# Kernel optimization log

Measured on AMD Instinct MI355X. Metric: run time of the kernel, lower is better.

## Reference

```python
import jax, jax.numpy as jnp
import numpy as np

N = 32768   # nodes
E = 524288  # edges (avg degree 16)
D = 128     # in_channels == num_hidden_channels
H = 4       # attention heads
C = D // H  # per-head out channels
R = 5       # num_relations
BS = 8192   # batch_size (output rows)
NEG = 0.2   # GATv2Conv leaky_relu negative slope


def segment_softmax(alpha, dst, n):
    amax = jax.lax.stop_gradient(jax.ops.segment_max(alpha, dst, num_segments=n))
    amax = jnp.where(jnp.isfinite(amax), amax, 0.0)
    a = jnp.exp(alpha - amax[dst])
    denom = jax.ops.segment_sum(a, dst, num_segments=n)
    return a / (denom[dst] + 1e-16)


def rel_edge_features(x, src, dst, Rmat, etype):
    # cat(src, dst) @ R[etype], computed per-relation to avoid gathering [E,2D,D]
    e = jnp.concatenate([x[src], x[dst]], axis=1)  # [E, 2D]
    out = jnp.zeros((e.shape[0], Rmat.shape[-1]), e.dtype)
    for r in range(Rmat.shape[0]):
        out = out + jnp.where((etype == r)[:, None], e @ Rmat[r], 0.0)
    return jax.nn.gelu(out, approximate=False)


def gatv2_conv(x, src, dst, edge_attr, Wl, bl, We, att, bias):
    # share_weights=True: x_l == x_r
    n = x.shape[0]
    xl = (x @ Wl + bl).reshape(n, H, C)
    m = xl[src] + xl[dst] + (edge_attr @ We).reshape(-1, H, C)  # [E,H,C]
    alpha = jnp.einsum('ehc,hc->eh', jax.nn.leaky_relu(m, NEG), att)
    alpha = segment_softmax(alpha, dst, n)
    msg = xl[src] * alpha[..., None]
    return jax.ops.segment_sum(msg, dst, num_segments=n).reshape(n, H * C) + bias


def setup_inputs():
    key = jax.random.key(0)
    ks = jax.random.split(key, 18)
    s = 0.05
    f32 = jnp.float32
    return {
        'embs': jax.random.normal(ks[0], (N, D), f32),
        'edge_index': jax.random.randint(ks[1], (2, E), 0, N),
        'edge_type': jax.random.randint(ks[2], (E,), 0, R),
        'rel_matrices': jax.random.normal(ks[3], (1, 2, R, 2 * D, D), f32) * s,
        'lin_l_w0': jax.random.normal(ks[4], (D, H * C), f32) * s,
        'lin_l_b0': jnp.zeros((H * C,), f32),
        'lin_edge_w0': jax.random.normal(ks[5], (D, H * C), f32) * s,
        'att0': jax.random.normal(ks[6], (H, C), f32) * s,
        'bias0': jnp.zeros((H * C,), f32),
        'lin_l_w1': jax.random.normal(ks[7], (D, H * C), f32) * s,
        'lin_l_b1': jnp.zeros((H * C,), f32),
        'lin_edge_w1': jax.random.normal(ks[8], (D, H * C), f32) * s,
        'att1': jax.random.normal(ks[9], (H, C), f32) * s,
        'bias1': jnp.zeros((H * C,), f32),
        'out_w': jax.random.normal(ks[10], (D, D), f32) * s,
        'out_b': jnp.zeros((D,), f32),
        'ln_g': jnp.ones((D,), f32),
        'ln_b': jnp.zeros((D,), f32),
        'batch_size': BS,
    }


def reference(embs, edge_index, edge_type, rel_matrices,
              lin_l_w0, lin_l_b0, lin_edge_w0, att0, bias0,
              lin_l_w1, lin_l_b1, lin_edge_w1, att1, bias1,
              out_w, out_b, ln_g, ln_b, batch_size):
    src, dst = edge_index[0], edge_index[1]
    x = embs
    # inner layer 0 (dropout no-op in eval)
    ea = rel_edge_features(x, src, dst, rel_matrices[0, 0], edge_type)
    x = gatv2_conv(x, src, dst, ea, lin_l_w0, lin_l_b0, lin_edge_w0, att0, bias0)
    x = jax.nn.gelu(x, approximate=False)
    # inner layer 1 (last -> no activation)
    ea = rel_edge_features(x, src, dst, rel_matrices[0, 1], edge_type)
    x = gatv2_conv(x, src, dst, ea, lin_l_w1, lin_l_b1, lin_edge_w1, att1, bias1)
    # output head: Linear -> LayerNorm(eps=1e-12) -> Dropout(no-op)
    y = x[:batch_size] @ out_w + out_b
    mu = y.mean(-1, keepdims=True)
    var = y.var(-1, keepdims=True)
    return (y - mu) / jnp.sqrt(var + 1e-12) * ln_g + ln_b
```

## Files before the change

### kernel.cpp

```cpp
#include <hip/hip_runtime.h>
#include <hip/hip_bf16.h>

typedef __hip_bfloat16 bf16;
typedef __attribute__((ext_vector_type(8))) short s8v;
typedef __attribute__((ext_vector_type(4))) float f4v;
typedef __attribute__((ext_vector_type(2))) float f2v;
typedef unsigned short u16;
typedef unsigned int u32;
typedef unsigned char u8;
typedef long long i64;

#define NN 32768
#define NE 524288
#define D 128
#define H 4
#define C 32
#define R 5
#define BS 8192

__device__ __forceinline__ u16 f2bs(float x) { bf16 h = __float2bfloat16(x); return *(u16*)&h; }
__device__ __forceinline__ float bflo(u32 u) { return __uint_as_float(u << 16); }
__device__ __forceinline__ float bfhi(u32 u) { return __uint_as_float(u & 0xffff0000u); }
__device__ __forceinline__ u32 pack2r(float a, float b) {
    u32 ua = __float_as_uint(a) + 0x8000u;
    u32 ub = __float_as_uint(b) + 0x8000u;
    return __builtin_amdgcn_perm(ub, ua, 0x07060302u);
}
__device__ __forceinline__ u16 rnd16(float a) {
    return (u16)((__float_as_uint(a) + 0x8000u) >> 16);
}
__device__ __forceinline__ float gelu_f(float x) {
    return 0.5f * x * (1.f + erff(x * 0.7071067811865475f));
}
__device__ __forceinline__ f2v gelu_pk(f2v x) {
    f2v t;
    t.x = fminf(fmaxf(x.x, -4.f), 4.f);
    t.y = fminf(fmaxf(x.y, -4.f), 4.f);
    f2v s = t * t;
    f2v h = __builtin_elementwise_fma(s, (f2v)1.53421e-5f, (f2v)-7.13918e-4f);
    h = __builtin_elementwise_fma(s, h, (f2v)0.0129194f);
    h = __builtin_elementwise_fma(s, h, (f2v)-0.1207967f);
    h = __builtin_elementwise_fma(s, h, (f2v)0.794118f);
    f2v e = t * h;
    f2v hx = x * 0.5f;
    return __builtin_elementwise_fma(hx, e, hx);
}
template <int CTRL>
__device__ __forceinline__ float dpp_add(float v) {
    int t = __builtin_amdgcn_update_dpp(0, __float_as_int(v), CTRL, 0xf, 0xf, true);
    return v + __int_as_float(t);
}
__device__ __forceinline__ float rsum16(float v) {
    v = dpp_add<0x128>(v);
    v = dpp_add<0x124>(v);
    v = dpp_add<0x122>(v);
    v = dpp_add<0x121>(v);
    return v;
}

__device__ u16      g_x[NN * D];
__device__ float    g_araw[NE * H];
__device__ u8       g_P8[R * NN * D];
__device__ u8       g_Q8[R * NN * D];
__device__ u16      g_xl[NN * D];
__device__ u8       g_xl8[NN * D];
__device__ u16      g_WnF[26 * 2048 * 8];
__device__ int      g_cnt[NN];
__device__ int      g_cur[NN];
__device__ int      g_off[NN + 1];
__device__ int      g_se[NE];
__device__ int      g_de[NE];
__device__ int      g_re[NE];

__global__ void k_cvt(const float* __restrict__ e) {
    int i = blockIdx.x * 256 + threadIdx.x;
    float2 v = *(const float2*)&e[(size_t)i * 2];
    ((u32*)g_x)[i] = pack2r(v.x, v.y);
}

__global__ void k_zcnt() {
    int i = blockIdx.x * 256 + threadIdx.x;
    g_cnt[i] = 0; g_cur[i] = 0;
}
__global__ void k_count(const int* __restrict__ ei) {
    int i = blockIdx.x * 256 + threadIdx.x;
    atomicAdd(&g_cnt[ei[NE + i]], 1);
}
__global__ void k_scan() {
    __shared__ int sums[1024];
    const int t = threadIdx.x;
    const int base = t * 32;
    int local[32];
    int s = 0;
#pragma unroll
    for (int i = 0; i < 32; ++i) { local[i] = s; s += g_cnt[base + i]; }
    sums[t] = s;
    __syncthreads();
    for (int off = 1; off < 1024; off <<= 1) {
        int v = (t >= off) ? sums[t - off] : 0;
        __syncthreads();
        sums[t] += v;
        __syncthreads();
    }
    int chunkoff = (t == 0) ? 0 : sums[t - 1];
#pragma unroll
    for (int i = 0; i < 32; ++i) g_off[base + i] = chunkoff + local[i];
    if (t == 1023) g_off[NN] = sums[1023];
}
__global__ void k_scatter(const int* __restrict__ ei, const int* __restrict__ et) {
    int i = blockIdx.x * 256 + threadIdx.x;
    int d = ei[NE + i];
    int pos = g_off[d] + atomicAdd(&g_cur[d], 1);
    g_se[pos] = ei[i];
    g_de[pos] = d;
    g_re[pos] = et[i];
}

__global__ void k_prep(const float* __restrict__ Wl, const float* __restrict__ Rm,
                       const float* __restrict__ We, const float* __restrict__ Ow,
                       int base) {
    int f = blockIdx.x * 256 + threadIdx.x;
    int y = blockIdx.y;
    const float* src;
    if (y == 0) src = Wl;
    else if (y <= R) src = Rm + (size_t)(y - 1) * 2 * D * D;
    else if (y <= 2 * R) src = Rm + (size_t)(y - 1 - R) * 2 * D * D + D * D;
    else if (y == 11) src = We;
    else src = Ow;
    int lane = f & 63, nt = (f >> 6) & 7, s = f >> 9;
    int n = nt * 16 + (lane & 15);
    int ks = s * 32 + (lane >> 4) * 8;
    u16 tmp[8];
#pragma unroll
    for (int j = 0; j < 8; ++j) tmp[j] = f2bs(src[(size_t)(ks + j) * D + n]);
    *(uint4*)&g_WnF[((size_t)(base + y) * 2048 + f) * 8] = *(uint4*)tmp;
}

__global__ __launch_bounds__(256) void k_node(const float* __restrict__ bl, int wbase) {
    const int tid = threadIdx.x;
    const int n0 = blockIdx.x * 64;
    const int wstart = blockIdx.y * 3;
    const int wend = (wstart + 3 < 11) ? wstart + 3 : 11;
    const int l = tid & 63, w = tid >> 6;
    const int mrow = l & 15, quad = l >> 4;
    const u16* xrow = g_x + (size_t)(n0 + w * 16 + mrow) * D;

    s8v a[4];
#pragma unroll
    for (int s = 0; s < 4; ++s) a[s] = *(const s8v*)&xrow[s * 32 + quad * 8];

    for (int wsel = wstart; wsel < wend; ++wsel) {
        const u16* BF = g_WnF + (size_t)(wbase + wsel) * 2048 * 8;
        f4v acc[8];
#pragma unroll
        for (int nt = 0; nt < 8; ++nt) acc[nt] = (f4v){0.f, 0.f, 0.f, 0.f};
#pragma unroll
        for (int s = 0; s < 4; ++s) {
#pragma unroll
            for (int nt = 0; nt < 8; ++nt) {
                s8v b = *(const s8v*)&BF[(size_t)((s * 8 + nt) * 64 + l) * 8];
                acc[nt] = __builtin_amdgcn_mfma_f32_16x16x32_bf16(a[s], b, acc[nt], 0, 0, 0);
            }
        }

        if (wsel == 0) {
#pragma unroll
            for (int nt = 0; nt < 8; ++nt) {
                int col = nt * 16 + mrow;
                float bias = bl[col];
                float v[4];
#pragma unroll
                for (int r = 0; r < 4; ++r) v[r] = acc[nt][r] + bias;
#pragma unroll
                for (int r = 0; r < 4; ++r) {
                    int row = n0 + w * 16 + quad * 4 + r;
                    g_xl[(size_t)row * D + col] = rnd16(v[r]);
                }
#pragma unroll
                for (int r = 0; r < 4; r += 2) {
                    u32 pk = __builtin_amdgcn_cvt_pk_fp8_f32(v[r], v[r + 1], 0, false);
                    int row = n0 + w * 16 + quad * 4 + r;
                    g_xl8[(size_t)row * D + col] = (u8)(pk & 0xffu);
                    g_xl8[(size_t)(row + 1) * D + col] = (u8)((pk >> 8) & 0xffu);
                }
            }
        } else {
            u8* out8 = (wsel <= R) ? g_P8 + (size_t)(wsel - 1) * NN * D
                                   : g_Q8 + (size_t)(wsel - 1 - R) * NN * D;
#pragma unroll
            for (int nt = 0; nt < 8; ++nt) {
                int col = nt * 16 + mrow;
#pragma unroll
                for (int r = 0; r < 4; r += 2) {
                    u32 pk = __builtin_amdgcn_cvt_pk_fp8_f32(acc[nt][r], acc[nt][r + 1], 0, false);
                    int row = n0 + w * 16 + quad * 4 + r;
                    out8[(size_t)row * D + col] = (u8)(pk & 0xffu);
                    out8[(size_t)(row + 1) * D + col] = (u8)((pk >> 8) & 0xffu);
                }
            }
        }
    }
}

__global__ __launch_bounds__(256) void k_edge(const float* __restrict__ att, int wbase) {
    const int tid = threadIdx.x;
    const int e0 = blockIdx.x * 64;
    const int l = tid & 63, w = tid >> 6;
    const int mrow = l & 15, quad = l >> 4;
    const int myrow = w * 16 + mrow;
    const u16* BF = g_WnF + (size_t)(wbase + 11) * 2048 * 8;

    const int se = g_se[e0 + myrow];
    const int de = g_de[e0 + myrow];
    const int re = g_re[e0 + myrow];

    const int pos8 = (mrow & 7) * 8;
    const i64 bev8 = (quad == (mrow >> 3))     ? (i64)(0x38LL << pos8) : 0LL;
    const i64 bod8 = (quad == 2 + (mrow >> 3)) ? (i64)(0x38LL << pos8) : 0LL;

    const u8* Prow = g_P8 + ((size_t)re * NN + se) * D;
    const u8* Qrow = g_Q8 + ((size_t)re * NN + de) * D;
    const u8* Xs = g_xl8 + (size_t)se * D;
    const u8* Xd = g_xl8 + (size_t)de * D;
    union { u32 u[4]; s8v v; } af[4];
    uint2 su[4], du[4];
#pragma unroll
    for (int s = 0; s < 4; ++s) {
        int c0 = s * 32 + quad * 8;
        uint2 pu = *(const uint2*)&Prow[c0];
        uint2 qu = *(const uint2*)&Qrow[c0];
        su[s] = *(const uint2*)&Xs[c0];
        du[s] = *(const uint2*)&Xd[c0];
        f2v pq0 = __builtin_amdgcn_cvt_pk_f32_fp8(pu.x, false) + __builtin_amdgcn_cvt_pk_f32_fp8(qu.x, false);
        f2v pq1 = __builtin_amdgcn_cvt_pk_f32_fp8(pu.x, true)  + __builtin_amdgcn_cvt_pk_f32_fp8(qu.x, true);
        f2v pq2 = __builtin_amdgcn_cvt_pk_f32_fp8(pu.y, false) + __builtin_amdgcn_cvt_pk_f32_fp8(qu.y, false);
        f2v pq3 = __builtin_amdgcn_cvt_pk_f32_fp8(pu.y, true)  + __builtin_amdgcn_cvt_pk_f32_fp8(qu.y, true);
        f2v g0 = gelu_pk(pq0), g1 = gelu_pk(pq1), g2 = gelu_pk(pq2), g3 = gelu_pk(pq3);
        af[s].u[0] = pack2r(g0.x, g0.y);
        af[s].u[1] = pack2r(g1.x, g1.y);
        af[s].u[2] = pack2r(g2.x, g2.y);
        af[s].u[3] = pack2r(g3.x, g3.y);
    }

    f4v acc[8];
#pragma unroll
    for (int nt = 0; nt < 8; ++nt) acc[nt] = (f4v){0.f, 0.f, 0.f, 0.f};
#pragma unroll
    for (int s = 0; s < 4; ++s) {
#pragma unroll
        for (int nt = 0; nt < 8; ++nt) {
            s8v b = *(const s8v*)&BF[(size_t)((s * 8 + nt) * 64 + l) * 8];
            acc[nt] = __builtin_amdgcn_mfma_f32_16x16x32_bf16(af[s].v, b, acc[nt], 0, 0, 0);
        }
        const i64 as = (i64)(((unsigned long long)su[s].y << 32) | su[s].x);
        const i64 ad = (i64)(((unsigned long long)du[s].y << 32) | du[s].x);
        acc[2 * s]     = __builtin_amdgcn_mfma_f32_16x16x32_fp8_fp8(as, bev8, acc[2 * s], 0, 0, 0);
        acc[2 * s]     = __builtin_amdgcn_mfma_f32_16x16x32_fp8_fp8(ad, bev8, acc[2 * s], 0, 0, 0);
        acc[2 * s + 1] = __builtin_amdgcn_mfma_f32_16x16x32_fp8_fp8(as, bod8, acc[2 * s + 1], 0, 0, 0);
        acc[2 * s + 1] = __builtin_amdgcn_mfma_f32_16x16x32_fp8_fp8(ad, bod8, acc[2 * s + 1], 0, 0, 0);
    }

    float hsum[4][4];
#pragma unroll
    for (int r = 0; r < 4; ++r)
#pragma unroll
        for (int h = 0; h < 4; ++h) hsum[r][h] = 0.f;
#pragma unroll
    for (int nt = 0; nt < 8; ++nt) {
        int col = nt * 16 + mrow;
        float av = att[col];
        int h = nt >> 1;
#pragma unroll
        for (int r = 0; r < 4; ++r) {
            float m = acc[nt][r];
            float lr = fmaxf(m, 0.2f * m);
            hsum[r][h] = fmaf(lr, av, hsum[r][h]);
        }
    }
#pragma unroll
    for (int r = 0; r < 4; ++r)
#pragma unroll
        for (int h = 0; h < 4; ++h) hsum[r][h] = rsum16(hsum[r][h]);
    if ((mrow & 3) == 0) {
        int r = mrow >> 2;
        float4 v = make_float4(__expf(fminf(hsum[r][0], 80.f)),
                               __expf(fminf(hsum[r][1], 80.f)),
                               __expf(fminf(hsum[r][2], 80.f)),
                               __expf(fminf(hsum[r][3], 80.f)));
        *(float4*)&g_araw[(size_t)(e0 + w * 16 + quad * 4 + r) * H] = v;
    }
}

__global__ __launch_bounds__(256) void k_gath(const float* __restrict__ bias,
                                              int do_gelu) {
    const int lane = threadIdx.x & 63;
    const int d = blockIdx.x * 4 + (threadIdx.x >> 6);
    const int off = g_off[d];
    const int deg = g_off[d + 1] - off;
    const int h = lane >> 4;

    const int* __restrict__ srcs = g_se + off;
    const float* __restrict__ ar = g_araw + (size_t)off * H + h;
    float a0 = 0.f, a1 = 0.f, dn = 0.f;
    int p = 0;
    for (; p + 8 <= deg; p += 8) {
        int ss[8];
#pragma unroll
        for (int j = 0; j < 8; ++j) ss[j] = srcs[p + j];
        u32 ww[8];
#pragma unroll
        for (int j = 0; j < 8; ++j) ww[j] = *(const u32*)&g_xl[(size_t)ss[j] * D + lane * 2];
        float cc[8];
#pragma unroll
        for (int j = 0; j < 8; ++j) cc[j] = ar[(p + j) * H];
#pragma unroll
        for (int j = 0; j < 8; ++j) {
            dn += cc[j];
            a0 = fmaf(bflo(ww[j]), cc[j], a0);
            a1 = fmaf(bfhi(ww[j]), cc[j], a1);
        }
    }
    for (; p + 4 <= deg; p += 4) {
        int s0 = srcs[p], s1 = srcs[p + 1], s2 = srcs[p + 2], s3 = srcs[p + 3];
        u32 w0 = *(const u32*)&g_xl[(size_t)s0 * D + lane * 2];
        u32 w1 = *(const u32*)&g_xl[(size_t)s1 * D + lane * 2];
        u32 w2 = *(const u32*)&g_xl[(size_t)s2 * D + lane * 2];
        u32 w3 = *(const u32*)&g_xl[(size_t)s3 * D + lane * 2];
        float c0 = ar[(p + 0) * H];
        float c1 = ar[(p + 1) * H];
        float c2 = ar[(p + 2) * H];
        float c3 = ar[(p + 3) * H];
        dn += (c0 + c1) + (c2 + c3);
        a0 = fmaf(bflo(w0), c0, a0); a1 = fmaf(bfhi(w0), c0, a1);
        a0 = fmaf(bflo(w1), c1, a0); a1 = fmaf(bfhi(w1), c1, a1);
        a0 = fmaf(bflo(w2), c2, a0); a1 = fmaf(bfhi(w2), c2, a1);
        a0 = fmaf(bflo(w3), c3, a0); a1 = fmaf(bfhi(w3), c3, a1);
    }
    for (; p < deg; ++p) {
        int s = srcs[p];
        u32 w = *(const u32*)&g_xl[(size_t)s * D + lane * 2];
        float cf = ar[p * H];
        dn += cf;
        a0 = fmaf(bflo(w), cf, a0);
        a1 = fmaf(bfhi(w), cf, a1);
    }
    const float inv = __builtin_amdgcn_rcpf(dn + 1e-16f);
    float v0 = a0 * inv + bias[lane * 2];
    float v1 = a1 * inv + bias[lane * 2 + 1];
    if (do_gelu) { v0 = gelu_f(v0); v1 = gelu_f(v1); }
    ((u32*)g_x)[(size_t)d * (D / 2) + lane] = pack2r(v0, v1);
}

__global__ __launch_bounds__(256) void k_head(const float* __restrict__ ob,
                                              const float* __restrict__ g,
                                              const float* __restrict__ b,
                                              float* __restrict__ out) {
    const int tid = threadIdx.x;
    const int r0 = blockIdx.x * 64;
    const int l = tid & 63, w = tid >> 6;
    const int mrow = l & 15, quad = l >> 4;
    const u16* xrow = g_x + (size_t)(r0 + w * 16 + mrow) * D;
    const u16* BF = g_WnF + (size_t)12 * 2048 * 8;

    f4v acc[8];
#pragma unroll
    for (int nt = 0; nt < 8; ++nt) acc[nt] = (f4v){0.f, 0.f, 0.f, 0.f};
#pragma unroll
    for (int s = 0; s < 4; ++s) {
        s8v a = *(const s8v*)&xrow[s * 32 + quad * 8];
#pragma unroll
        for (int nt = 0; nt < 8; ++nt) {
            s8v bb = *(const s8v*)&BF[(size_t)((s * 8 + nt) * 64 + l) * 8];
            acc[nt] = __builtin_amdgcn_mfma_f32_16x16x32_bf16(a, bb, acc[nt], 0, 0, 0);
        }
    }

    float sum[4] = {0.f, 0.f, 0.f, 0.f};
#pragma unroll
    for (int nt = 0; nt < 8; ++nt) {
        float obv = ob[nt * 16 + mrow];
#pragma unroll
        for (int r = 0; r < 4; ++r) {
            acc[nt][r] += obv;
            sum[r] += acc[nt][r];
        }
    }
    float mu[4];
#pragma unroll
    for (int r = 0; r < 4; ++r) mu[r] = rsum16(sum[r]) * (1.f / D);
    float sq[4] = {0.f, 0.f, 0.f, 0.f};
#pragma unroll
    for (int nt = 0; nt < 8; ++nt)
#pragma unroll
        for (int r = 0; r < 4; ++r) {
            float dv = acc[nt][r] - mu[r];
            sq[r] += dv * dv;
        }
    float rs[4];
#pragma unroll
    for (int r = 0; r < 4; ++r) rs[r] = rsqrtf(rsum16(sq[r]) * (1.f / D) + 1e-12f);
#pragma unroll
    for (int nt = 0; nt < 8; ++nt) {
        int col = nt * 16 + mrow;
        float gv = g[col], bv = b[col];
#pragma unroll
        for (int r = 0; r < 4; ++r) {
            int row = r0 + w * 16 + quad * 4 + r;
            out[(size_t)row * D + col] = (acc[nt][r] - mu[r]) * rs[r] * gv + bv;
        }
    }
}

extern "C" void kernel_launch(void* const* d_in, const int* in_sizes, int n_in,
                              void* d_out, int out_size, void* d_ws, size_t ws_size,
                              hipStream_t stream) {
    (void)in_sizes; (void)n_in; (void)out_size; (void)d_ws; (void)ws_size;
    const float* embs = (const float*)d_in[0];
    const int*   ei   = (const int*)d_in[1];
    const int*   et   = (const int*)d_in[2];
    const float* rel  = (const float*)d_in[3];
    const float* wl[2]   = { (const float*)d_in[4],  (const float*)d_in[9]  };
    const float* bl[2]   = { (const float*)d_in[5],  (const float*)d_in[10] };
    const float* we[2]   = { (const float*)d_in[6],  (const float*)d_in[11] };
    const float* attw[2] = { (const float*)d_in[7],  (const float*)d_in[12] };
    const float* bs[2]   = { (const float*)d_in[8],  (const float*)d_in[13] };
    const float* ow  = (const float*)d_in[14];
    const float* ob  = (const float*)d_in[15];
    const float* lng = (const float*)d_in[16];
    const float* lnb = (const float*)d_in[17];
    float* out = (float*)d_out;

    k_cvt<<<NN * D / 512, 256, 0, stream>>>(embs);

    for (int l = 0; l < 2; ++l) {
        const float* Rm = rel + (size_t)l * R * 2 * D * D;
        k_prep<<<dim3(2048 / 256, 13), 256, 0, stream>>>(wl[l], Rm, we[l], ow, l * 13);
    }

    k_zcnt<<<NN / 256, 256, 0, stream>>>();
    k_count<<<NE / 256, 256, 0, stream>>>(ei);
    k_scan<<<1, 1024, 0, stream>>>();
    k_scatter<<<NE / 256, 256, 0, stream>>>(ei, et);

    for (int l = 0; l < 2; ++l) {
        k_node<<<dim3(NN / 64, 4), 256, 0, stream>>>(bl[l], l * 13);
        k_edge<<<NE / 64, 256, 0, stream>>>(attw[l], l * 13);
        k_gath<<<NN / 4, 256, 0, stream>>>(bs[l], l == 0 ? 1 : 0);
    }

    k_head<<<BS / 64, 256, 0, stream>>>(ob, lng, lnb, out);
}
```

Measured before the change: 478.3 us.

## Sort edges by relation type before edge kernel for gather locality

Adds a stable counting sort that groups CSR-ordered edges by relation type: per-block histograms, a global scan, and a scatter that ranks edges within each block. The edge kernel then reads edges in relation-grouped order, so the P8/Q8 rows it gathers come from a single relation slab at a time. Scores are written back to their original CSR position through a packed index. This adds three small preprocessing kernels, including an O(256) per-thread rank loop, and an indirect scattered store of the attention scores, in exchange for better cache locality on the relation-table gathers.

Measured after the change: 491.9 us. +2.8%, slower.

```diff
diff --git a/kernel.cpp b/kernel.cpp
--- a/kernel.cpp
+++ b/kernel.cpp
@@ -17,6 +17,7 @@
 #define C 32
 #define R 5
 #define BS 8192
+#define NB 2048
 
 __device__ __forceinline__ u16 f2bs(float x) { bf16 h = __float2bfloat16(x); return *(u16*)&h; }
 __device__ __forceinline__ float bflo(u32 u) { return __uint_as_float(u << 16); }
@@ -71,6 +72,10 @@
 __device__ int      g_se[NE];
 __device__ int      g_de[NE];
 __device__ int      g_re[NE];
+__device__ int      g_bh[R * NB];
+__device__ int      g_hse[NE];
+__device__ int      g_hde[NE];
+__device__ u32      g_hpr[NE];
 
 __global__ void k_cvt(const float* __restrict__ e) {
     int i = blockIdx.x * 256 + threadIdx.x;
@@ -114,6 +119,52 @@
     g_se[pos] = ei[i];
     g_de[pos] = d;
     g_re[pos] = et[i];
+}
+
+__global__ void k_phist() {
+    __shared__ int h[R];
+    const int t = threadIdx.x, b = blockIdx.x;
+    if (t < R) h[t] = 0;
+    __syncthreads();
+    atomicAdd(&h[g_re[b * 256 + t]], 1);
+    __syncthreads();
+    if (t < R) g_bh[t * NB + b] = h[t];
+}
+__global__ void k_pscan() {
+    __shared__ int sums[1024];
+    const int t = threadIdx.x;
+    const int base = t * 10;
+    int local[10];
+    int s = 0;
+#pragma unroll
+    for (int i = 0; i < 10; ++i) { local[i] = s; s += g_bh[base + i]; }
+    sums[t] = s;
+    __syncthreads();
+    for (int off = 1; off < 1024; off <<= 1) {
+        int v = (t >= off) ? sums[t - off] : 0;
+        __syncthreads();
+        sums[t] += v;
+        __syncthreads();
+    }
+    int chunkoff = (t == 0) ? 0 : sums[t - 1];
+#pragma unroll
+    for (int i = 0; i < 10; ++i) g_bh[base + i] = chunkoff + local[i];
+}
+__global__ void k_pscat() {
+    __shared__ u8 lre[256];
+    __shared__ int bofs[R];
+    const int t = threadIdx.x, b = blockIdx.x;
+    const int i = b * 256 + t;
+    const int re = g_re[i];
+    lre[t] = (u8)re;
+    if (t < R) bofs[t] = g_bh[t * NB + b];
+    __syncthreads();
+    int rank = 0;
+    for (int j = 0; j < t; ++j) rank += (lre[j] == (u8)re);
+    const int pos = bofs[re] + rank;
+    g_hse[pos] = g_se[i];
+    g_hde[pos] = g_de[i];
+    g_hpr[pos] = ((u32)re << 24) | (u32)i;
 }
 
 __global__ void k_prep(const float* __restrict__ Wl, const float* __restrict__ Rm,
@@ -210,9 +261,9 @@
     const int myrow = w * 16 + mrow;
     const u16* BF = g_WnF + (size_t)(wbase + 11) * 2048 * 8;
 
-    const int se = g_se[e0 + myrow];
-    const int de = g_de[e0 + myrow];
-    const int re = g_re[e0 + myrow];
+    const int se = g_hse[e0 + myrow];
+    const int de = g_hde[e0 + myrow];
+    const int re = (int)(g_hpr[e0 + myrow] >> 24);
 
     const int pos8 = (mrow & 7) * 8;
     const i64 bev8 = (quad == (mrow >> 3))     ? (i64)(0x38LL << pos8) : 0LL;
@@ -283,11 +334,12 @@
         for (int h = 0; h < 4; ++h) hsum[r][h] = rsum16(hsum[r][h]);
     if ((mrow & 3) == 0) {
         int r = mrow >> 2;
+        int cpos = (int)(g_hpr[e0 + w * 16 + quad * 4 + r] & 0xFFFFFFu);
         float4 v = make_float4(__expf(fminf(hsum[r][0], 80.f)),
                                __expf(fminf(hsum[r][1], 80.f)),
                                __expf(fminf(hsum[r][2], 80.f)),
                                __expf(fminf(hsum[r][3], 80.f)));
-        *(float4*)&g_araw[(size_t)(e0 + w * 16 + quad * 4 + r) * H] = v;
+        *(float4*)&g_araw[(size_t)cpos * H] = v;
     }
 }
 
@@ -442,6 +494,10 @@
     k_scan<<<1, 1024, 0, stream>>>();
     k_scatter<<<NE / 256, 256, 0, stream>>>(ei, et);
 
+    k_phist<<<NB, 256, 0, stream>>>();
+    k_pscan<<<1, 1024, 0, stream>>>();
+    k_pscat<<<NB, 256, 0, stream>>>();
+
     for (int l = 0; l < 2; ++l) {
         k_node<<<dim3(NN / 64, 4), 256, 0, stream>>>(bl[l], l * 13);
         k_edge<<<NE / 64, 256, 0, stream>>>(attw[l], l * 13);
```
